# Performance work log

Measured on AMD Instinct MI355X. Metric: run time of the kernel, lower is better.

The kernel has to match this reference:

```python
import jax, jax.numpy as jnp
import numpy as np

B, E, K, S, D, H, C = 8192, 8, 2, 32, 3072, 256, 100  # batch, experts, fix_points, img size, flat dim, hidden, classes


def setup_inputs() -> dict:
    key = jax.random.key(0)
    ks = jax.random.split(key, 6)
    return {
        "x": jax.random.normal(ks[0], (B, 3, S, S), jnp.float32),
        "coeffs_t": jax.random.uniform(ks[1], (K,), jnp.float32),
        "router_w": jax.random.normal(ks[2], (K, D, E), jnp.float32) * 0.02,
        "router_b": jnp.zeros((K, E), jnp.float32),
        "w1": jax.random.normal(ks[3], (E, K, D, H), jnp.float32) * 0.02,
        "b1": jnp.zeros((E, K, H), jnp.float32),
        "w2": jax.random.normal(ks[4], (E, K, H, C), jnp.float32) * 0.02,
        "b2": jnp.zeros((E, K, C), jnp.float32),
    }


def reference(x, coeffs_t, router_w, router_b, w1, b1, w2, b2):
    xf = x.reshape(x.shape[0], -1)  # [B, D]
    # Curve parameter blend: W = sum_k coeffs_t[k] * W_k (CurveParameter semantics)
    Wr = jnp.einsum('k,kde->de', coeffs_t, router_w)
    br = jnp.einsum('k,ke->e', coeffs_t, router_b)
    # Router: top-1 expert index per sample
    idx = jnp.argmax(xf @ Wr + br, axis=-1)  # [B] int
    # Blended expert weights
    W1 = jnp.einsum('k,ekdh->edh', coeffs_t, w1)
    B1 = jnp.einsum('k,ekh->eh', coeffs_t, b1)
    W2 = jnp.einsum('k,ekhc->ehc', coeffs_t, w2)
    B2 = jnp.einsum('k,ekc->ec', coeffs_t, b2)
    # Expert MLP (computed for all experts with static shapes, then top-1 gather;
    # identical math to torch's boolean-mask dispatch/scatter)
    h = jax.nn.gelu(jnp.einsum('bd,edh->beh', xf, W1) + B1, approximate=False)  # [B,E,H]
    o = jnp.einsum('beh,ehc->bec', h, W2) + B2  # [B,E,C]
    return jnp.take_along_axis(o, idx[:, None, None], axis=1)[:, 0, :]  # [B,C]
```

## Files before the change

### kernel.cpp

```cpp
#include <hip/hip_runtime.h>
#include <math.h>

#define B_  8192
#define E_  8
#define D_  3072
#define H_  256
#define C_  100
#define DH_ (D_*H_)
#define HC_ (H_*C_)
#define KS_ 8
#define KSEG_ (D_/KS_)
#define NTMAX_ 136
#define NT2MAX_ 528

typedef __attribute__((ext_vector_type(4))) float  f32x4;
typedef __attribute__((ext_vector_type(8))) __bf16 bf16x8;
typedef __attribute__((ext_vector_type(8))) unsigned short ush8;
typedef __attribute__((ext_vector_type(4))) unsigned short ush4;

__device__ inline unsigned short bf16_rne(float f) {
    unsigned u = __builtin_bit_cast(unsigned, f);
    unsigned r = (u + 0x7FFFu + ((u >> 16) & 1u)) >> 16;
    return (unsigned short)r;
}
__device__ inline float bf16_f(unsigned short h) {
    unsigned u = ((unsigned)h) << 16;
    return __builtin_bit_cast(float, u);
}

#define MISC_B1_ (E_*H_/4)
#define MISC_B2_ (E_*C_/4)
#define MISC_TOT_ (MISC_B1_ + MISC_B2_ + D_)
__global__ __launch_bounds__(256) void blend_misc_k(
        const float* __restrict__ b1, const float* __restrict__ b2,
        const float* __restrict__ rw, float* __restrict__ B1b,
        float* __restrict__ B2b, double* __restrict__ wsd,
        const float* __restrict__ coeffs) {
    int gid = blockIdx.x * 256 + threadIdx.x;
    float c0 = coeffs[0], c1 = coeffs[1];
    if (gid < MISC_B1_) {
        const float4* p = (const float4*)b1;
        int e = gid / (H_ / 4), r = gid - e * (H_ / 4);
        float4 a = p[(e * 2 + 0) * (H_ / 4) + r];
        float4 bq = p[(e * 2 + 1) * (H_ / 4) + r];
        float4 o;
        o.x = c0 * a.x + c1 * bq.x;
        o.y = c0 * a.y + c1 * bq.y;
        o.z = c0 * a.z + c1 * bq.z;
        o.w = c0 * a.w + c1 * bq.w;
        ((float4*)B1b)[gid] = o;
    } else if (gid < MISC_B1_ + MISC_B2_) {
        int g2 = gid - MISC_B1_;
        const float4* p = (const float4*)b2;
        int e = g2 / (C_ / 4), r = g2 - e * (C_ / 4);
        float4 a = p[(e * 2 + 0) * (C_ / 4) + r];
        float4 bq = p[(e * 2 + 1) * (C_ / 4) + r];
        float4 o;
        o.x = c0 * a.x + c1 * bq.x;
        o.y = c0 * a.y + c1 * bq.y;
        o.z = c0 * a.z + c1 * bq.z;
        o.w = c0 * a.w + c1 * bq.w;
        ((float4*)B2b)[g2] = o;
    } else {
        int d = gid - (MISC_B1_ + MISC_B2_);
        if (d < D_) {
            double c0d = (double)c0, c1d = (double)c1;
            #pragma unroll
            for (int ee = 0; ee < 8; ee++)
                wsd[(size_t)d * 8 + ee] = c0d * (double)rw[(size_t)d * 8 + ee]
                                        + c1d * (double)rw[(size_t)(D_ + d) * 8 + ee];
        }
    }
}

#define TP_ 136
__global__ __launch_bounds__(256) void blendw1t_k(
        const float* __restrict__ w1, unsigned short* __restrict__ Whi,
        unsigned short* __restrict__ Wlo, const float* __restrict__ coeffs) {
    __shared__ unsigned short thi[64 * TP_];
    __shared__ unsigned short tlo[64 * TP_];
    float c0 = coeffs[0], c1 = coeffs[1];
    int t = threadIdx.x;
    int e = blockIdx.z, h0 = blockIdx.y * 64, d0 = blockIdx.x * 128;
    int h = t & 63, dl = t >> 6;
    const float* pa = w1 + ((size_t)(e * 2 + 0) * D_ + d0) * H_ + h0 + h;
    const float* pb = w1 + ((size_t)(e * 2 + 1) * D_ + d0) * H_ + h0 + h;
    for (int it = 0; it < 32; it++) {
        int d = it * 4 + dl;
        float v = c0 * pa[(size_t)d * H_] + c1 * pb[(size_t)d * H_];
        unsigned short hi = bf16_rne(v);
        thi[h * TP_ + d] = hi;
        tlo[h * TP_ + d] = bf16_rne(v - bf16_f(hi));
    }
    __syncthreads();
    #pragma unroll
    for (int it = 0; it < 4; it++) {
        int i = t + it * 256;
        int hh = i >> 4, d8 = (i & 15) * 8;
        size_t g = (size_t)(e * H_ + h0 + hh) * D_ + d0 + d8;
        *(ush8*)(Whi + g) = *(const ush8*)&thi[hh * TP_ + d8];
        *(ush8*)(Wlo + g) = *(const ush8*)&tlo[hh * TP_ + d8];
    }
}

__global__ __launch_bounds__(256) void blendw2t_k(
        const float* __restrict__ w2, unsigned short* __restrict__ W2thi,
        unsigned short* __restrict__ W2tlo, const float* __restrict__ coeffs) {
    float c0 = coeffs[0], c1 = coeffs[1];
    int c = blockIdx.x, e = blockIdx.y, k = threadIdx.x;
    float v = c0 * w2[((size_t)(e * 2 + 0) * H_ + k) * C_ + c]
            + c1 * w2[((size_t)(e * 2 + 1) * H_ + k) * C_ + c];
    unsigned short hi = bf16_rne(v);
    W2thi[(size_t)(e * C_ + c) * H_ + k] = hi;
    W2tlo[(size_t)(e * C_ + c) * H_ + k] = bf16_rne(v - bf16_f(hi));
}

template<int RKS>
__global__ __launch_bounds__(64) void router_v2_t(
        const float* __restrict__ x, const double* __restrict__ wsd,
        double* __restrict__ lpart) {
    const int RSEG = D_ / RKS;
    __shared__ float  xs[64][33];
    __shared__ double wls[32][8];
    int lane = threadIdx.x;
    int row0 = blockIdx.x * 64;
    int kbase = blockIdx.y * RSEG;

    double acc[8] = {0, 0, 0, 0, 0, 0, 0, 0};

    for (int kb = 0; kb < RSEG; kb += 32) {
        #pragma unroll
        for (int it = 0; it < 8; it++) {
            int i = lane + it * 64;
            int r = i >> 3, c4 = i & 7;
            *(float4*)&xs[r][c4 * 4] =
                *(const float4*)(x + (size_t)(row0 + r) * D_ + kbase + kb + c4 * 4);
        }
        #pragma unroll
        for (int it = 0; it < 4; it++) {
            int i = lane + it * 64;
            int k = i >> 3, ee = i & 7;
            wls[k][ee] = wsd[(size_t)(kbase + kb + k) * 8 + ee];
        }
        __syncthreads();
        #pragma unroll
        for (int kk = 0; kk < 32; kk++) {
            double xv = (double)xs[lane][kk];
            double2 w01 = *(const double2*)&wls[kk][0];
            double2 w23 = *(const double2*)&wls[kk][2];
            double2 w45 = *(const double2*)&wls[kk][4];
            double2 w67 = *(const double2*)&wls[kk][6];
            acc[0] = fma(xv, w01.x, acc[0]);
            acc[1] = fma(xv, w01.y, acc[1]);
            acc[2] = fma(xv, w23.x, acc[2]);
            acc[3] = fma(xv, w23.y, acc[3]);
            acc[4] = fma(xv, w45.x, acc[4]);
            acc[5] = fma(xv, w45.y, acc[5]);
            acc[6] = fma(xv, w67.x, acc[6]);
            acc[7] = fma(xv, w67.y, acc[7]);
        }
        __syncthreads();
    }
    size_t base = ((size_t)blockIdx.y * B_ + row0 + lane) * 8;
    #pragma unroll
    for (int ee = 0; ee < 8; ee++) lpart[base + ee] = acc[ee];
}

template<int RKS>
__global__ __launch_bounds__(256) void argmax_t(
        const double* __restrict__ lpart, const float* __restrict__ rb,
        const float* __restrict__ coeffs, int* __restrict__ idx,
        int* __restrict__ cnt) {
    __shared__ int scnt[8];
    int t = threadIdx.x;
    if (t < 8) scnt[t] = 0;
    __syncthreads();
    int b = blockIdx.x * 256 + t;
    double c0 = (double)coeffs[0], c1 = (double)coeffs[1];
    double best = -1e300;
    int bi = 0;
    #pragma unroll
    for (int e = 0; e < 8; e++) {
        double l = c0 * (double)rb[e] + c1 * (double)rb[8 + e];
        #pragma unroll
        for (int s2 = 0; s2 < RKS; s2++)
            l += lpart[((size_t)s2 * B_ + b) * 8 + e];
        if (l > best) { best = l; bi = e; }
    }
    idx[b] = bi;
    atomicAdd(&scnt[bi], 1);
    __syncthreads();
    if (t < 8 && scnt[t] > 0) atomicAdd(&cnt[t], scnt[t]);
}

__global__ void offsets_k(const int* __restrict__ cnt, int* __restrict__ off,
                          int* __restrict__ cursor, int* __restrict__ tmap,
                          int* __restrict__ tmap2, int* __restrict__ ntl) {
    if (threadIdx.x == 0) {
        int s = 0;
        for (int e = 0; e < E_; e++) { off[e] = s; cursor[e] = s; s += cnt[e]; }
        int nt = 0;
        for (int e = 0; e < E_; e++)
            for (int t0 = 0; t0 < cnt[e]; t0 += 64)
                tmap[nt++] = (e << 16) | t0;
        ntl[0] = nt;
        int nt2 = 0;
        for (int e = 0; e < E_; e++)
            for (int t0 = 0; t0 < cnt[e]; t0 += 16)
                tmap2[nt2++] = (e << 16) | t0;
        ntl[1] = nt2;
    }
}

__global__ void scatter_k(const int* __restrict__ idx, int* __restrict__ cursor,
                          int* __restrict__ order) {
    int b = blockIdx.x * blockDim.x + threadIdx.x;
    if (b < B_) {
        int e = idx[b];
        int pos = atomicAdd(&cursor[e], 1);
        order[pos] = (e << 16) | b;
    }
}

template<int MODE>
__global__ __launch_bounds__(256, 3) void gemm1_t(
        const float* __restrict__ x, const unsigned short* __restrict__ Whi,
        const unsigned short* __restrict__ Wlo, const int* __restrict__ order,
        const int* __restrict__ cnt, const int* __restrict__ off,
        const int* __restrict__ tmap, const int* __restrict__ ntl,
        float* __restrict__ dst) {
    int tid = blockIdx.y;
    if (tid >= ntl[0]) return;
    int tm = tmap[tid];
    int e = tm >> 16, tile0 = tm & 0xFFFF;
    int ce = cnt[e];
    int s = blockIdx.x;

    __shared__ int rows[64];
    __shared__ unsigned short xs_hi[64 * 40];
    __shared__ unsigned short xs_lo[64 * 40];
    __shared__ unsigned short ws_hi[256 * 40];
    __shared__ unsigned short ws_lo[256 * 40];

    int t = threadIdx.x;
    if (t < 64) {
        int i = tile0 + t;
        rows[t] = (i < ce) ? (order[off[e] + i] & 0xFFFF) : -1;
    }
    __syncthreads();
    int xrow0 = rows[0];

    int lane = t & 63, w = t >> 6;
    int lr = lane & 15, quad = lane >> 4;
    int kbase = s * KSEG_;

    f32x4 acc[4][4];
    #pragma unroll
    for (int mt = 0; mt < 4; mt++)
        #pragma unroll
        for (int nt = 0; nt < 4; nt++)
            acc[mt][nt] = (f32x4){0.f, 0.f, 0.f, 0.f};

    for (int kb = 0; kb < KSEG_; kb += 32) {
        #pragma unroll
        for (int it = 0; it < 2; it++) {
            int i = t + it * 256;
            int rr = i >> 3, sg = i & 7;
            int row = rows[rr];
            if (row < 0) row = xrow0;
            float4 v = *(const float4*)(x + (size_t)row * D_ + kbase + kb + sg * 4);
            unsigned short h4[4], l4[4];
            float vv[4] = {v.x, v.y, v.z, v.w};
            #pragma unroll
            for (int j = 0; j < 4; j++) {
                unsigned short hi = bf16_rne(vv[j]);
                h4[j] = hi;
                l4[j] = bf16_rne(vv[j] - bf16_f(hi));
            }
            *(ush4*)&xs_hi[rr * 40 + sg * 4] = *(const ush4*)h4;
            *(ush4*)&xs_lo[rr * 40 + sg * 4] = *(const ush4*)l4;
        }
        #pragma unroll
        for (int it = 0; it < 4; it++) {
            int i = t + it * 256;
            int col = i >> 2, ch = i & 3;
            size_t g = (size_t)(e * H_ + col) * D_ + kbase + kb + ch * 8;
            *(ush8*)&ws_hi[col * 40 + ch * 8] = *(const ush8*)(Whi + g);
            *(ush8*)&ws_lo[col * 40 + ch * 8] = *(const ush8*)(Wlo + g);
        }
        __syncthreads();

        bf16x8 ah[4], al[4], bh[4], bl[4];
        #pragma unroll
        for (int mt = 0; mt < 4; mt++) {
            ah[mt] = __builtin_bit_cast(bf16x8, *(const ush8*)&xs_hi[(mt * 16 + lr) * 40 + quad * 8]);
            al[mt] = __builtin_bit_cast(bf16x8, *(const ush8*)&xs_lo[(mt * 16 + lr) * 40 + quad * 8]);
        }
        #pragma unroll
        for (int nt = 0; nt < 4; nt++) {
            int col = w * 64 + nt * 16 + lr;
            bh[nt] = __builtin_bit_cast(bf16x8, *(const ush8*)&ws_hi[col * 40 + quad * 8]);
            bl[nt] = __builtin_bit_cast(bf16x8, *(const ush8*)&ws_lo[col * 40 + quad * 8]);
        }
        #pragma unroll
        for (int mt = 0; mt < 4; mt++)
            #pragma unroll
            for (int nt = 0; nt < 4; nt++) {
                acc[mt][nt] = __builtin_amdgcn_mfma_f32_16x16x32_bf16(ah[mt], bh[nt], acc[mt][nt], 0, 0, 0);
                acc[mt][nt] = __builtin_amdgcn_mfma_f32_16x16x32_bf16(al[mt], bh[nt], acc[mt][nt], 0, 0, 0);
                acc[mt][nt] = __builtin_amdgcn_mfma_f32_16x16x32_bf16(ah[mt], bl[nt], acc[mt][nt], 0, 0, 0);
                acc[mt][nt] = __builtin_amdgcn_mfma_f32_16x16x32_bf16(al[mt], bl[nt], acc[mt][nt], 0, 0, 0);
            }
        __syncthreads();
    }

    size_t p0 = (size_t)off[e] + tile0;
    if (MODE == 1) {
        float* dp = dst + ((size_t)s * B_ + p0) * H_;
        #pragma unroll
        for (int mt = 0; mt < 4; mt++) {
            int rl = mt * 16 + quad * 4;
            #pragma unroll
            for (int nt = 0; nt < 4; nt++) {
                int col = w * 64 + nt * 16 + lr;
                #pragma unroll
                for (int rg = 0; rg < 4; rg++) {
                    if (tile0 + rl + rg < ce)
                        dp[(size_t)(rl + rg) * H_ + col] = acc[mt][nt][rg];
                }
            }
        }
    } else {
        #pragma unroll
        for (int mt = 0; mt < 4; mt++) {
            int rl = mt * 16 + quad * 4;
            #pragma unroll
            for (int nt = 0; nt < 4; nt++) {
                int col = w * 64 + nt * 16 + lr;
                #pragma unroll
                for (int rg = 0; rg < 4; rg++) {
                    if (tile0 + rl + rg < ce)
                        atomicAdd(&dst[(p0 + rl + rg) * H_ + col], acc[mt][nt][rg]);
                }
            }
        }
    }
}

__global__ __launch_bounds__(256) void bias_gelu_k(
        float* __restrict__ hws, const float* __restrict__ B1b,
        const int* __restrict__ order) {
    int gid = blockIdx.x * 256 + threadIdx.x;
    int p = gid >> 6, c4 = (gid & 63) * 4;
    int e = order[p] >> 16;
    float4 v = *(const float4*)(hws + (size_t)p * H_ + c4);
    const float4 bb = *(const float4*)(B1b + e * H_ + c4);
    float pre[4] = {v.x + bb.x, v.y + bb.y, v.z + bb.z, v.w + bb.w};
    float4 o;
    o.x = 0.5f * pre[0] * (1.0f + erff(pre[0] * 0.70710678118654752440f));
    o.y = 0.5f * pre[1] * (1.0f + erff(pre[1] * 0.70710678118654752440f));
    o.z = 0.5f * pre[2] * (1.0f + erff(pre[2] * 0.70710678118654752440f));
    o.w = 0.5f * pre[3] * (1.0f + erff(pre[3] * 0.70710678118654752440f));
    *(float4*)(hws + (size_t)p * H_ + c4) = o;
}

template<int FUSE>
__global__ __launch_bounds__(256) void gemm2_t(
        const float* __restrict__ hsrc,
        const unsigned short* __restrict__ W2thi, const unsigned short* __restrict__ W2tlo,
        const float* __restrict__ B1b, const float* __restrict__ B2b,
        const int* __restrict__ order, const int* __restrict__ cnt,
        const int* __restrict__ off, const int* __restrict__ tmap2,
        const int* __restrict__ ntl, float* __restrict__ out) {
    int tid = blockIdx.x;
    if (tid >= ntl[1]) return;
    int tm = tmap2[tid];
    int e = tm >> 16, tile0 = tm & 0xFFFF;
    int ce = cnt[e];

    __shared__ int rows[16];
    __shared__ float red[3][64][28];

    int t = threadIdx.x;
    if (t < 16) {
        int i = tile0 + t;
        rows[t] = (i < ce) ? (order[off[e] + i] & 0xFFFF) : -1;
    }
    __syncthreads();

    int lane = t & 63, w = t >> 6;
    int m = lane & 15, q = lane >> 4;
    int p = off[e] + tile0 + ((tile0 + m < ce) ? m : 0);

    f32x4 acc[7];
    #pragma unroll
    for (int nt = 0; nt < 7; nt++) acc[nt] = (f32x4){0.f, 0.f, 0.f, 0.f};

    const unsigned short* w2h = W2thi + (size_t)e * C_ * H_;
    const unsigned short* w2l = W2tlo + (size_t)e * C_ * H_;

    #pragma unroll
    for (int si = 0; si < 2; si++) {
        int s = w * 2 + si;
        int k0 = s * 32 + q * 8;
        size_t o = (size_t)p * H_ + k0;
        float f[8];
        if (FUSE) {
            float4 a0 = *(const float4*)(hsrc + o);
            float4 a1 = *(const float4*)(hsrc + o + 4);
            #pragma unroll
            for (int s2 = 1; s2 < KS_; s2++) {
                const float* sp = hsrc + (size_t)s2 * B_ * H_ + o;
                float4 b0 = *(const float4*)sp;
                float4 b1v = *(const float4*)(sp + 4);
                a0.x += b0.x; a0.y += b0.y; a0.z += b0.z; a0.w += b0.w;
                a1.x += b1v.x; a1.y += b1v.y; a1.z += b1v.z; a1.w += b1v.w;
            }
            float4 bb0 = *(const float4*)(B1b + e * H_ + k0);
            float4 bb1 = *(const float4*)(B1b + e * H_ + k0 + 4);
            float pre[8] = {a0.x + bb0.x, a0.y + bb0.y, a0.z + bb0.z, a0.w + bb0.w,
                            a1.x + bb1.x, a1.y + bb1.y, a1.z + bb1.z, a1.w + bb1.w};
            #pragma unroll
            for (int j = 0; j < 8; j++)
                f[j] = 0.5f * pre[j] * (1.0f + erff(pre[j] * 0.70710678118654752440f));
        } else {
            float4 v0 = *(const float4*)(hsrc + o);
            float4 v1 = *(const float4*)(hsrc + o + 4);
            f[0] = v0.x; f[1] = v0.y; f[2] = v0.z; f[3] = v0.w;
            f[4] = v1.x; f[5] = v1.y; f[6] = v1.z; f[7] = v1.w;
        }
        unsigned short hh[8], lo[8];
        #pragma unroll
        for (int j = 0; j < 8; j++) {
            unsigned short hi = bf16_rne(f[j]);
            hh[j] = hi;
            lo[j] = bf16_rne(f[j] - bf16_f(hi));
        }
        bf16x8 ah = __builtin_bit_cast(bf16x8, *(const ush8*)hh);
        bf16x8 al = __builtin_bit_cast(bf16x8, *(const ush8*)lo);
        #pragma unroll
        for (int nt = 0; nt < 7; nt++) {
            size_t bo = (size_t)(nt * 16 + m) * H_ + k0;
            bf16x8 bh = __builtin_bit_cast(bf16x8, *(const ush8*)(w2h + bo));
            bf16x8 bl = __builtin_bit_cast(bf16x8, *(const ush8*)(w2l + bo));
            acc[nt] = __builtin_amdgcn_mfma_f32_16x16x32_bf16(ah, bh, acc[nt], 0, 0, 0);
            acc[nt] = __builtin_amdgcn_mfma_f32_16x16x32_bf16(al, bh, acc[nt], 0, 0, 0);
            acc[nt] = __builtin_amdgcn_mfma_f32_16x16x32_bf16(ah, bl, acc[nt], 0, 0, 0);
            acc[nt] = __builtin_amdgcn_mfma_f32_16x16x32_bf16(al, bl, acc[nt], 0, 0, 0);
        }
    }

    if (w > 0) {
        #pragma unroll
        for (int nt = 0; nt < 7; nt++)
            #pragma unroll
            for (int i = 0; i < 4; i++)
                red[w - 1][lane][nt * 4 + i] = acc[nt][i];
    }
    __syncthreads();
    if (w == 0) {
        #pragma unroll
        for (int nt = 0; nt < 7; nt++)
            #pragma unroll
            for (int i = 0; i < 4; i++)
                acc[nt][i] = ((acc[nt][i] + red[0][lane][nt * 4 + i])
                              + red[1][lane][nt * 4 + i]) + red[2][lane][nt * 4 + i];
        #pragma unroll
        for (int nt = 0; nt < 7; nt++) {
            int c = nt * 16 + m;
            if (c >= C_) continue;
            float bias = B2b[e * C_ + c];
            #pragma unroll
            for (int i = 0; i < 4; i++) {
                int grow = q * 4 + i;
                if (tile0 + grow < ce)
                    out[(size_t)rows[grow] * C_ + c] = acc[nt][i] + bias;
            }
        }
    }
}

extern "C" void kernel_launch(void* const* d_in, const int* in_sizes, int n_in,
                              void* d_out, int out_size, void* d_ws, size_t ws_size,
                              hipStream_t stream) {
    const float* x        = (const float*)d_in[0];
    const float* coeffs   = (const float*)d_in[1];
    const float* router_w = (const float*)d_in[2];
    const float* router_b = (const float*)d_in[3];
    const float* w1       = (const float*)d_in[4];
    const float* b1       = (const float*)d_in[5];
    const float* w2       = (const float*)d_in[6];
    const float* b2       = (const float*)d_in[7];
    float* out = (float*)d_out;

    unsigned short* Whi   = (unsigned short*)d_ws;
    unsigned short* Wlo   = Whi + (size_t)E_ * DH_;
    unsigned short* W2thi = Wlo + (size_t)E_ * DH_;
    unsigned short* W2tlo = W2thi + (size_t)E_ * C_ * H_;
    float* B1b  = (float*)(W2tlo + (size_t)E_ * C_ * H_);
    float* B2b  = B1b + (size_t)E_ * H_;
    int* order  = (int*)(B2b + E_ * C_);
    int* cnt    = order + B_;
    int* off    = cnt + E_;
    int* cursor = off + E_;
    int* tmap   = cursor + E_;
    int* tmap2  = tmap + NTMAX_;
    int* ntl    = tmap2 + NT2MAX_;
    float* hws  = (float*)(ntl + 4);

    size_t prefix_bytes = (size_t)((char*)hws - (char*)d_ws);
    int use_part = (ws_size >= prefix_bytes + (size_t)KS_ * B_ * H_ * sizeof(float) + 256) ? 1 : 0;

    hipMemsetAsync(cnt, 0, 3 * E_ * sizeof(int), stream);

    blendw1t_k<<<dim3(D_ / 128, H_ / 64, E_), 256, 0, stream>>>(w1, Whi, Wlo, coeffs);
    blendw2t_k<<<dim3(C_, E_), 256, 0, stream>>>(w2, W2thi, W2tlo, coeffs);

    if (use_part) {
        double* lpart = (double*)hws;
        double* wsd   = (double*)(hws + (size_t)B_ * H_);
        int*    idx   = (int*)((char*)(hws + (size_t)B_ * H_) + (1u << 20));

        blend_misc_k<<<dim3((MISC_TOT_ + 255) / 256), 256, 0, stream>>>(
            b1, b2, router_w, B1b, B2b, wsd, coeffs);
        router_v2_t<16><<<dim3(B_ / 64, 16), 64, 0, stream>>>(x, wsd, lpart);
        argmax_t<16><<<dim3(B_ / 256), 256, 0, stream>>>(lpart, router_b, coeffs, idx, cnt);
        offsets_k<<<1, 64, 0, stream>>>(cnt, off, cursor, tmap, tmap2, ntl);
        scatter_k<<<dim3(B_ / 256), 256, 0, stream>>>(idx, cursor, order);

        gemm1_t<1><<<dim3(KS_, NTMAX_), 256, 0, stream>>>(x, Whi, Wlo, order, cnt,
                                                          off, tmap, ntl, hws);
        gemm2_t<1><<<dim3(NT2MAX_), 256, 0, stream>>>(hws, W2thi, W2tlo, B1b, B2b,
                                                      order, cnt, off, tmap2, ntl, out);
    } else {
        double* lpart = (double*)hws;
        double* wsd   = (double*)((char*)hws + (size_t)8 * B_ * 8 * 8);
        int*    idx   = (int*)((char*)hws + (5u << 20));

        blend_misc_k<<<dim3((MISC_TOT_ + 255) / 256), 256, 0, stream>>>(
            b1, b2, router_w, B1b, B2b, wsd, coeffs);
        router_v2_t<8><<<dim3(B_ / 64, 8), 64, 0, stream>>>(x, wsd, lpart);
        argmax_t<8><<<dim3(B_ / 256), 256, 0, stream>>>(lpart, router_b, coeffs, idx, cnt);
        offsets_k<<<1, 64, 0, stream>>>(cnt, off, cursor, tmap, tmap2, ntl);
        scatter_k<<<dim3(B_ / 256), 256, 0, stream>>>(idx, cursor, order);

        hipMemsetAsync(hws, 0, (size_t)B_ * H_ * sizeof(float), stream);
        gemm1_t<0><<<dim3(KS_, NTMAX_), 256, 0, stream>>>(x, Whi, Wlo, order, cnt,
                                                          off, tmap, ntl, hws);
        bias_gelu_k<<<dim3(B_ * H_ / 4 / 256), 256, 0, stream>>>(hws, B1b, order);
        gemm2_t<0><<<dim3(NT2MAX_), 256, 0, stream>>>(hws, W2thi, W2tlo, B1b, B2b,
                                                      order, cnt, off, tmap2, ntl, out);
    }
}
```

Measured before the change: 366.4 us.

## Fuse router, weight blends and bias blends into one heterogeneous kernel

```diff
diff --git a/kernel.cpp b/kernel.cpp
--- a/kernel.cpp
+++ b/kernel.cpp
@@ -10,8 +10,17 @@
 #define HC_ (H_*C_)
 #define KS_ 8
 #define KSEG_ (D_/KS_)
+#define RKS_ 16
+#define RSEG_ (D_/RKS_)
+#define RB_ (B_/256)
 #define NTMAX_ 136
 #define NT2MAX_ 528
+
+#define MEGA_R_   (RB_*RKS_)
+#define MEGA_W1_  (24*4*8)
+#define MEGA_W2_  (C_*E_)
+#define MEGA_BB_  3
+#define MEGA_TOT_ (MEGA_R_ + MEGA_W1_ + MEGA_W2_ + MEGA_BB_)
 
 typedef __attribute__((ext_vector_type(4))) float  f32x4;
 typedef __attribute__((ext_vector_type(8))) __bf16 bf16x8;
@@ -30,144 +39,143 @@
 
 #define MISC_B1_ (E_*H_/4)
 #define MISC_B2_ (E_*C_/4)
-#define MISC_TOT_ (MISC_B1_ + MISC_B2_ + D_)
-__global__ __launch_bounds__(256) void blend_misc_k(
+
+__global__ __launch_bounds__(256) void mega_k(
+        const float* __restrict__ x, const float* __restrict__ rw,
+        const float* __restrict__ w1, const float* __restrict__ w2,
         const float* __restrict__ b1, const float* __restrict__ b2,
-        const float* __restrict__ rw, float* __restrict__ B1b,
-        float* __restrict__ B2b, double* __restrict__ wsd,
-        const float* __restrict__ coeffs) {
-    int gid = blockIdx.x * 256 + threadIdx.x;
-    float c0 = coeffs[0], c1 = coeffs[1];
-    if (gid < MISC_B1_) {
-        const float4* p = (const float4*)b1;
-        int e = gid / (H_ / 4), r = gid - e * (H_ / 4);
-        float4 a = p[(e * 2 + 0) * (H_ / 4) + r];
-        float4 bq = p[(e * 2 + 1) * (H_ / 4) + r];
-        float4 o;
-        o.x = c0 * a.x + c1 * bq.x;
-        o.y = c0 * a.y + c1 * bq.y;
-        o.z = c0 * a.z + c1 * bq.z;
-        o.w = c0 * a.w + c1 * bq.w;
-        ((float4*)B1b)[gid] = o;
-    } else if (gid < MISC_B1_ + MISC_B2_) {
-        int g2 = gid - MISC_B1_;
-        const float4* p = (const float4*)b2;
-        int e = g2 / (C_ / 4), r = g2 - e * (C_ / 4);
-        float4 a = p[(e * 2 + 0) * (C_ / 4) + r];
-        float4 bq = p[(e * 2 + 1) * (C_ / 4) + r];
-        float4 o;
-        o.x = c0 * a.x + c1 * bq.x;
-        o.y = c0 * a.y + c1 * bq.y;
-        o.z = c0 * a.z + c1 * bq.z;
-        o.w = c0 * a.w + c1 * bq.w;
-        ((float4*)B2b)[g2] = o;
+        unsigned short* __restrict__ Whi, unsigned short* __restrict__ Wlo,
+        unsigned short* __restrict__ W2thi, unsigned short* __restrict__ W2tlo,
+        float* __restrict__ B1b, float* __restrict__ B2b,
+        double* __restrict__ lpart, const float* __restrict__ coeffs) {
+    __shared__ char smem[36864];
+    int bid = blockIdx.x;
+    int t = threadIdx.x;
+
+    if (bid < MEGA_R_) {
+        float  (*xs)[64][33] = (float(*)[64][33])smem;
+        double (*wls)[8]     = (double(*)[8])(smem + 33792);
+        int w = t >> 6, lane = t & 63;
+        int rowblk = (bid & (RB_ - 1)) * 256;
+        int s2     = bid >> 5;
+        int kbase  = s2 * RSEG_;
+        int row0   = rowblk + w * 64;
+        double c0 = (double)coeffs[0], c1 = (double)coeffs[1];
+
+        double acc[8] = {0, 0, 0, 0, 0, 0, 0, 0};
+
+        for (int kb = 0; kb < RSEG_; kb += 32) {
+            #pragma unroll
+            for (int it = 0; it < 8; it++) {
+                int i = lane + it * 64;
+                int r = i >> 3, c4 = i & 7;
+                *(float4*)&xs[w][r][c4 * 4] =
+                    *(const float4*)(x + (size_t)(row0 + r) * D_ + kbase + kb + c4 * 4);
+            }
+            if (w == 0) {
+                #pragma unroll
+                for (int it = 0; it < 4; it++) {
+                    int i = lane + it * 64;
+                    int k = i >> 3, ee = i & 7;
+                    wls[k][ee] = c0 * (double)rw[(size_t)(kbase + kb + k) * 8 + ee]
+                               + c1 * (double)rw[(size_t)(D_ + kbase + kb + k) * 8 + ee];
+                }
+            }
+            __syncthreads();
+            #pragma unroll
+            for (int kk = 0; kk < 32; kk++) {
+                double xv = (double)xs[w][lane][kk];
+                double2 w01 = *(const double2*)&wls[kk][0];
+                double2 w23 = *(const double2*)&wls[kk][2];
+                double2 w45 = *(const double2*)&wls[kk][4];
+                double2 w67 = *(const double2*)&wls[kk][6];
+                acc[0] = fma(xv, w01.x, acc[0]);
+                acc[1] = fma(xv, w01.y, acc[1]);
+                acc[2] = fma(xv, w23.x, acc[2]);
+                acc[3] = fma(xv, w23.y, acc[3]);
+                acc[4] = fma(xv, w45.x, acc[4]);
+                acc[5] = fma(xv, w45.y, acc[5]);
+                acc[6] = fma(xv, w67.x, acc[6]);
+                acc[7] = fma(xv, w67.y, acc[7]);
+            }
+            __syncthreads();
+        }
+        size_t base = ((size_t)s2 * B_ + row0 + lane) * 8;
+        #pragma unroll
+        for (int ee = 0; ee < 8; ee++) lpart[base + ee] = acc[ee];
+
+    } else if (bid < MEGA_R_ + MEGA_W1_) {
+        int lid = bid - MEGA_R_;
+        int e  = lid / 96;
+        int r  = lid - e * 96;
+        int h0 = (r / 24) * 64;
+        int d0 = (r % 24) * 128;
+        const int TP = 136;
+        unsigned short* thi = (unsigned short*)smem;
+        unsigned short* tlo = thi + 64 * TP;
+        float c0 = coeffs[0], c1 = coeffs[1];
+        int h = t & 63, dl = t >> 6;
+        const float* pa = w1 + ((size_t)(e * 2 + 0) * D_ + d0) * H_ + h0 + h;
+        const float* pb = w1 + ((size_t)(e * 2 + 1) * D_ + d0) * H_ + h0 + h;
+        for (int it = 0; it < 32; it++) {
+            int d = it * 4 + dl;
+            float v = c0 * pa[(size_t)d * H_] + c1 * pb[(size_t)d * H_];
+            unsigned short hi = bf16_rne(v);
+            thi[h * TP + d] = hi;
+            tlo[h * TP + d] = bf16_rne(v - bf16_f(hi));
+        }
+        __syncthreads();
+        #pragma unroll
+        for (int it = 0; it < 4; it++) {
+            int i = t + it * 256;
+            int hh = i >> 4, d8 = (i & 15) * 8;
+            size_t g = (size_t)(e * H_ + h0 + hh) * D_ + d0 + d8;
+            *(ush8*)(Whi + g) = *(const ush8*)&thi[hh * TP + d8];
+            *(ush8*)(Wlo + g) = *(const ush8*)&tlo[hh * TP + d8];
+        }
+
+    } else if (bid < MEGA_R_ + MEGA_W1_ + MEGA_W2_) {
+        int lid = bid - (MEGA_R_ + MEGA_W1_);
+        int c = lid % C_, e = lid / C_;
+        int k = t;
+        float c0 = coeffs[0], c1 = coeffs[1];
+        float v = c0 * w2[((size_t)(e * 2 + 0) * H_ + k) * C_ + c]
+                + c1 * w2[((size_t)(e * 2 + 1) * H_ + k) * C_ + c];
+        unsigned short hi = bf16_rne(v);
+        W2thi[(size_t)(e * C_ + c) * H_ + k] = hi;
+        W2tlo[(size_t)(e * C_ + c) * H_ + k] = bf16_rne(v - bf16_f(hi));
+
     } else {
-        int d = gid - (MISC_B1_ + MISC_B2_);
-        if (d < D_) {
-            double c0d = (double)c0, c1d = (double)c1;
-            #pragma unroll
-            for (int ee = 0; ee < 8; ee++)
-                wsd[(size_t)d * 8 + ee] = c0d * (double)rw[(size_t)d * 8 + ee]
-                                        + c1d * (double)rw[(size_t)(D_ + d) * 8 + ee];
-        }
-    }
-}
-
-#define TP_ 136
-__global__ __launch_bounds__(256) void blendw1t_k(
-        const float* __restrict__ w1, unsigned short* __restrict__ Whi,
-        unsigned short* __restrict__ Wlo, const float* __restrict__ coeffs) {
-    __shared__ unsigned short thi[64 * TP_];
-    __shared__ unsigned short tlo[64 * TP_];
-    float c0 = coeffs[0], c1 = coeffs[1];
-    int t = threadIdx.x;
-    int e = blockIdx.z, h0 = blockIdx.y * 64, d0 = blockIdx.x * 128;
-    int h = t & 63, dl = t >> 6;
-    const float* pa = w1 + ((size_t)(e * 2 + 0) * D_ + d0) * H_ + h0 + h;
-    const float* pb = w1 + ((size_t)(e * 2 + 1) * D_ + d0) * H_ + h0 + h;
-    for (int it = 0; it < 32; it++) {
-        int d = it * 4 + dl;
-        float v = c0 * pa[(size_t)d * H_] + c1 * pb[(size_t)d * H_];
-        unsigned short hi = bf16_rne(v);
-        thi[h * TP_ + d] = hi;
-        tlo[h * TP_ + d] = bf16_rne(v - bf16_f(hi));
-    }
-    __syncthreads();
-    #pragma unroll
-    for (int it = 0; it < 4; it++) {
-        int i = t + it * 256;
-        int hh = i >> 4, d8 = (i & 15) * 8;
-        size_t g = (size_t)(e * H_ + h0 + hh) * D_ + d0 + d8;
-        *(ush8*)(Whi + g) = *(const ush8*)&thi[hh * TP_ + d8];
-        *(ush8*)(Wlo + g) = *(const ush8*)&tlo[hh * TP_ + d8];
-    }
-}
-
-__global__ __launch_bounds__(256) void blendw2t_k(
-        const float* __restrict__ w2, unsigned short* __restrict__ W2thi,
-        unsigned short* __restrict__ W2tlo, const float* __restrict__ coeffs) {
-    float c0 = coeffs[0], c1 = coeffs[1];
-    int c = blockIdx.x, e = blockIdx.y, k = threadIdx.x;
-    float v = c0 * w2[((size_t)(e * 2 + 0) * H_ + k) * C_ + c]
-            + c1 * w2[((size_t)(e * 2 + 1) * H_ + k) * C_ + c];
-    unsigned short hi = bf16_rne(v);
-    W2thi[(size_t)(e * C_ + c) * H_ + k] = hi;
-    W2tlo[(size_t)(e * C_ + c) * H_ + k] = bf16_rne(v - bf16_f(hi));
-}
-
-template<int RKS>
-__global__ __launch_bounds__(64) void router_v2_t(
-        const float* __restrict__ x, const double* __restrict__ wsd,
-        double* __restrict__ lpart) {
-    const int RSEG = D_ / RKS;
-    __shared__ float  xs[64][33];
-    __shared__ double wls[32][8];
-    int lane = threadIdx.x;
-    int row0 = blockIdx.x * 64;
-    int kbase = blockIdx.y * RSEG;
-
-    double acc[8] = {0, 0, 0, 0, 0, 0, 0, 0};
-
-    for (int kb = 0; kb < RSEG; kb += 32) {
-        #pragma unroll
-        for (int it = 0; it < 8; it++) {
-            int i = lane + it * 64;
-            int r = i >> 3, c4 = i & 7;
-            *(float4*)&xs[r][c4 * 4] =
-                *(const float4*)(x + (size_t)(row0 + r) * D_ + kbase + kb + c4 * 4);
-        }
-        #pragma unroll
-        for (int it = 0; it < 4; it++) {
-            int i = lane + it * 64;
-            int k = i >> 3, ee = i & 7;
-            wls[k][ee] = wsd[(size_t)(kbase + kb + k) * 8 + ee];
-        }
-        __syncthreads();
-        #pragma unroll
-        for (int kk = 0; kk < 32; kk++) {
-            double xv = (double)xs[lane][kk];
-            double2 w01 = *(const double2*)&wls[kk][0];
-            double2 w23 = *(const double2*)&wls[kk][2];
-            double2 w45 = *(const double2*)&wls[kk][4];
-            double2 w67 = *(const double2*)&wls[kk][6];
-            acc[0] = fma(xv, w01.x, acc[0]);
-            acc[1] = fma(xv, w01.y, acc[1]);
-            acc[2] = fma(xv, w23.x, acc[2]);
-            acc[3] = fma(xv, w23.y, acc[3]);
-            acc[4] = fma(xv, w45.x, acc[4]);
-            acc[5] = fma(xv, w45.y, acc[5]);
-            acc[6] = fma(xv, w67.x, acc[6]);
-            acc[7] = fma(xv, w67.y, acc[7]);
-        }
-        __syncthreads();
-    }
-    size_t base = ((size_t)blockIdx.y * B_ + row0 + lane) * 8;
-    #pragma unroll
-    for (int ee = 0; ee < 8; ee++) lpart[base + ee] = acc[ee];
-}
-
-template<int RKS>
-__global__ __launch_bounds__(256) void argmax_t(
+        int gid = (bid - (MEGA_R_ + MEGA_W1_ + MEGA_W2_)) * 256 + t;
+        float c0 = coeffs[0], c1 = coeffs[1];
+        if (gid < MISC_B1_) {
+            const float4* p = (const float4*)b1;
+            int e = gid / (H_ / 4), r = gid - e * (H_ / 4);
+            float4 a = p[(e * 2 + 0) * (H_ / 4) + r];
+            float4 bq = p[(e * 2 + 1) * (H_ / 4) + r];
+            float4 o;
+            o.x = c0 * a.x + c1 * bq.x;
+            o.y = c0 * a.y + c1 * bq.y;
+            o.z = c0 * a.z + c1 * bq.z;
+            o.w = c0 * a.w + c1 * bq.w;
+            ((float4*)B1b)[gid] = o;
+        } else if (gid < MISC_B1_ + MISC_B2_) {
+            int g2 = gid - MISC_B1_;
+            const float4* p = (const float4*)b2;
+            int e = g2 / (C_ / 4), r = g2 - e * (C_ / 4);
+            float4 a = p[(e * 2 + 0) * (C_ / 4) + r];
+            float4 bq = p[(e * 2 + 1) * (C_ / 4) + r];
+            float4 o;
+            o.x = c0 * a.x + c1 * bq.x;
+            o.y = c0 * a.y + c1 * bq.y;
+            o.z = c0 * a.z + c1 * bq.z;
+            o.w = c0 * a.w + c1 * bq.w;
+            ((float4*)B2b)[g2] = o;
+        }
+    }
+}
+
+__global__ __launch_bounds__(256) void argmax_k(
         const double* __restrict__ lpart, const float* __restrict__ rb,
         const float* __restrict__ coeffs, int* __restrict__ idx,
         int* __restrict__ cnt) {
@@ -177,16 +185,21 @@
     __syncthreads();
     int b = blockIdx.x * 256 + t;
     double c0 = (double)coeffs[0], c1 = (double)coeffs[1];
+    double l[8];
+    #pragma unroll
+    for (int e = 0; e < 8; e++)
+        l[e] = c0 * (double)rb[e] + c1 * (double)rb[8 + e];
+    for (int s2 = 0; s2 < RKS_; s2++) {
+        const double2* pp = (const double2*)(lpart + ((size_t)s2 * B_ + b) * 8);
+        double2 v0 = pp[0], v1 = pp[1], v2 = pp[2], v3 = pp[3];
+        l[0] += v0.x; l[1] += v0.y; l[2] += v1.x; l[3] += v1.y;
+        l[4] += v2.x; l[5] += v2.y; l[6] += v3.x; l[7] += v3.y;
+    }
     double best = -1e300;
     int bi = 0;
     #pragma unroll
-    for (int e = 0; e < 8; e++) {
-        double l = c0 * (double)rb[e] + c1 * (double)rb[8 + e];
-        #pragma unroll
-        for (int s2 = 0; s2 < RKS; s2++)
-            l += lpart[((size_t)s2 * B_ + b) * 8 + e];
-        if (l > best) { best = l; bi = e; }
-    }
+    for (int e = 0; e < 8; e++)
+        if (l[e] > best) { best = l[e]; bi = e; }
     idx[b] = bi;
     atomicAdd(&scnt[bi], 1);
     __syncthreads();
@@ -506,44 +519,29 @@
     int* tmap   = cursor + E_;
     int* tmap2  = tmap + NTMAX_;
     int* ntl    = tmap2 + NT2MAX_;
-    float* hws  = (float*)(ntl + 4);
+    int* idx    = ntl + 4;
+    float* hws  = (float*)(idx + B_);
+    double* lpart = (double*)hws;
 
     size_t prefix_bytes = (size_t)((char*)hws - (char*)d_ws);
     int use_part = (ws_size >= prefix_bytes + (size_t)KS_ * B_ * H_ * sizeof(float) + 256) ? 1 : 0;
 
     hipMemsetAsync(cnt, 0, 3 * E_ * sizeof(int), stream);
 
-    blendw1t_k<<<dim3(D_ / 128, H_ / 64, E_), 256, 0, stream>>>(w1, Whi, Wlo, coeffs);
-    blendw2t_k<<<dim3(C_, E_), 256, 0, stream>>>(w2, W2thi, W2tlo, coeffs);
+    mega_k<<<dim3(MEGA_TOT_), 256, 0, stream>>>(
+        x, router_w, w1, w2, b1, b2, Whi, Wlo, W2thi, W2tlo, B1b, B2b,
+        lpart, coeffs);
+
+    argmax_k<<<dim3(B_ / 256), 256, 0, stream>>>(lpart, router_b, coeffs, idx, cnt);
+    offsets_k<<<1, 64, 0, stream>>>(cnt, off, cursor, tmap, tmap2, ntl);
+    scatter_k<<<dim3(B_ / 256), 256, 0, stream>>>(idx, cursor, order);
 
     if (use_part) {
-        double* lpart = (double*)hws;
-        double* wsd   = (double*)(hws + (size_t)B_ * H_);
-        int*    idx   = (int*)((char*)(hws + (size_t)B_ * H_) + (1u << 20));
-
-        blend_misc_k<<<dim3((MISC_TOT_ + 255) / 256), 256, 0, stream>>>(
-            b1, b2, router_w, B1b, B2b, wsd, coeffs);
-        router_v2_t<16><<<dim3(B_ / 64, 16), 64, 0, stream>>>(x, wsd, lpart);
-        argmax_t<16><<<dim3(B_ / 256), 256, 0, stream>>>(lpart, router_b, coeffs, idx, cnt);
-        offsets_k<<<1, 64, 0, stream>>>(cnt, off, cursor, tmap, tmap2, ntl);
-        scatter_k<<<dim3(B_ / 256), 256, 0, stream>>>(idx, cursor, order);
-
         gemm1_t<1><<<dim3(KS_, NTMAX_), 256, 0, stream>>>(x, Whi, Wlo, order, cnt,
                                                           off, tmap, ntl, hws);
         gemm2_t<1><<<dim3(NT2MAX_), 256, 0, stream>>>(hws, W2thi, W2tlo, B1b, B2b,
                                                       order, cnt, off, tmap2, ntl, out);
     } else {
-        double* lpart = (double*)hws;
-        double* wsd   = (double*)((char*)hws + (size_t)8 * B_ * 8 * 8);
-        int*    idx   = (int*)((char*)hws + (5u << 20));
-
-        blend_misc_k<<<dim3((MISC_TOT_ + 255) / 256), 256, 0, stream>>>(
-            b1, b2, router_w, B1b, B2b, wsd, coeffs);
-        router_v2_t<8><<<dim3(B_ / 64, 8), 64, 0, stream>>>(x, wsd, lpart);
-        argmax_t<8><<<dim3(B_ / 256), 256, 0, stream>>>(lpart, router_b, coeffs, idx, cnt);
-        offsets_k<<<1, 64, 0, stream>>>(cnt, off, cursor, tmap, tmap2, ntl);
-        scatter_k<<<dim3(B_ / 256), 256, 0, stream>>>(idx, cursor, order);
-
         hipMemsetAsync(hws, 0, (size_t)B_ * H_ * sizeof(float), stream);
         gemm1_t<0><<<dim3(KS_, NTMAX_), 256, 0, stream>>>(x, Whi, Wlo, order, cnt,
                                                           off, tmap, ntl, hws);
```

Result: faster. 358.8 us (-2.1%).
